# Performance work log

Hardware: AMD Instinct MI355X
Metric: run time of the kernel (lower is better)

The kernel has to match this reference:

```python
import jax, jax.numpy as jnp
import numpy as np

B, T = 8, 1024
C_IN, C_H = 4096, 4096
K_I, K_H = 3, 3
INIT_SPARSITY = 0.15


def _fixed_fanin_bipartite(rng, n_out, n_in, k):
    # exactly k True entries per row, distinct columns
    r = rng.random((n_out, n_in))
    cols = np.argsort(r, axis=1)[:, :k]
    A = np.zeros((n_out, n_in), np.float32)
    np.put_along_axis(A, cols, 1.0, axis=1)
    return A


def _fixed_fanin_graph(rng, n, k):
    # exactly k True entries per row, distinct non-self columns
    r = rng.random((n, n))
    np.fill_diagonal(r, 2.0)  # exclude self-loops
    cols = np.argsort(r, axis=1)[:, :k]
    A = np.zeros((n, n), np.float32)
    np.put_along_axis(A, cols, 1.0, axis=1)
    return A


def setup_inputs() -> dict:
    rng = np.random.default_rng(0)
    z = jnp.asarray(rng.random((B, T, C_IN)) < INIT_SPARSITY)          # bool (B,T,C_in)
    h0 = jnp.asarray(rng.random((B, C_H)) < INIT_SPARSITY)             # bool (B,C_h)
    A_input_f = jnp.asarray(_fixed_fanin_bipartite(rng, C_H, C_IN, K_I))  # (C_h,C_in) f32
    A_hidden_f = jnp.asarray(_fixed_fanin_graph(rng, C_H, K_H))           # (C_h,C_h) f32
    return {"z": z, "h0": h0, "A_input_f": A_input_f, "A_hidden_f": A_hidden_f}


def reference(z, h0, A_input_f, A_hidden_f):
    # AND-of-ORs CA: h_i(t) = [OR over input fan-in of z(t)] AND [OR over hidden fan-in of h(t-1)]
    z_tf = jnp.moveaxis(z, -2, 0)  # (T, B, C_in)

    def step(h, z_t):
        input_or = (z_t.astype(jnp.float32) @ A_input_f.T) > 0   # (B, C_h) bool
        hidden_or = (h.astype(jnp.float32) @ A_hidden_f.T) > 0   # (B, C_h) bool
        h_new = input_or & hidden_or
        return h_new, h_new

    _, h_seq = jax.lax.scan(step, h0, z_tf)   # (T, B, C_h)
    h_seq = jnp.moveaxis(h_seq, 0, -2)        # (B, T, C_h)
    return jnp.concatenate([z, h_seq], axis=-1)  # (B, T, C_in + C_h) bool
```

## Files before the change

### kernel.cpp

```cpp
#include <hip/hip_runtime.h>
#include <stdint.h>

#define B_   8
#define T_   1024
#define CIN_ 4096
#define CH_  4096
#define GRP  16
#define NGRP (T_ / GRP)


__device__ __forceinline__ uint32_t bytes_nonzero01(uint32_t w) {
  uint32_t t = (w & 0x7F7F7F7Fu) + 0x7F7F7F7Fu;
  t = (t | w) & 0x80808080u;
  return t >> 7;
}

__device__ __forceinline__ uint32_t load4(const void* base, long idx4, int es) {
  if (es == 1) {
    uint32_t w = ((const uint32_t*)base)[idx4];
    return bytes_nonzero01(w);
  } else if (es == 2) {
    uint32_t w0 = ((const uint32_t*)base)[idx4 * 2];
    uint32_t w1 = ((const uint32_t*)base)[idx4 * 2 + 1];
    uint32_t r = 0;
    r |= ((w0 & 0xFFFFu) != 0u) ? 0x00000001u : 0u;
    r |= ((w0 >> 16)     != 0u) ? 0x00000100u : 0u;
    r |= ((w1 & 0xFFFFu) != 0u) ? 0x00010000u : 0u;
    r |= ((w1 >> 16)     != 0u) ? 0x01000000u : 0u;
    return r;
  } else {
    uint4 w = ((const uint4*)base)[idx4];
    uint32_t r = 0;
    r |= (w.x != 0u) ? 0x00000001u : 0u;
    r |= (w.y != 0u) ? 0x00000100u : 0u;
    r |= (w.z != 0u) ? 0x00010000u : 0u;
    r |= (w.w != 0u) ? 0x01000000u : 0u;
    return r;
  }
}

__device__ __forceinline__ uint4 expand01(uint32_t v4) {
  uint4 r = { v4 & 1u, (v4 >> 8) & 1u, (v4 >> 16) & 1u, (v4 >> 24) & 1u };
  return r;
}

__device__ __forceinline__ void wait_ge(uint32_t* p, uint32_t tgt) {
  while (__hip_atomic_load(p, __ATOMIC_RELAXED, __HIP_MEMORY_SCOPE_AGENT) < tgt)
    __builtin_amdgcn_s_sleep(2);
  __threadfence();
}
__device__ __forceinline__ void bump(uint32_t* p) {
  __threadfence();
  __hip_atomic_fetch_add(p, 1u, __ATOMIC_RELAXED, __HIP_MEMORY_SCOPE_AGENT);
}

#define BID_DETECT 8
#define BID_EXTIN0 9
#define BID_EXTH0  265
#define BID_INOR0  521
#define NBLK       (521 + T_)

__global__ __launch_bounds__(1024) void mega_kernel(const void* __restrict__ z,
                                                    const void* __restrict__ h0,
                                                    const float* __restrict__ Ain,
                                                    const float* __restrict__ Ah,
                                                    uint32_t* __restrict__ modep,
                                                    uint32_t* __restrict__ idxin,
                                                    uint32_t* __restrict__ idxh,
                                                    uint32_t* __restrict__ inorb,
                                                    uint32_t* __restrict__ flags,
                                                    uint32_t* __restrict__ out) {
  __shared__ __align__(16) unsigned char smem[88 * 1024];
  unsigned char* sm0 = &smem[0];
  unsigned char* sm1 = &smem[4096];
  int* scnt = (int*)&smem[8192];
  const int bid = blockIdx.x;
  const int n = threadIdx.x;

  if (bid < 8) {
    __builtin_amdgcn_s_setprio(1);
    const int b = bid;
    if (n == 0) wait_ge(&flags[0], 1);
    __syncthreads();
    const int es = (int)modep[0];
    ((uint32_t*)sm0)[n] = load4(h0, (long)b * 1024 + n, es);
    if (n == 0) wait_ge(&flags[2], 256);
    __syncthreads();
    uint32_t d[4][3];
    {
      const uint4* p = (const uint4*)(idxh + n * 12);
      uint4 q0 = p[0], q1 = p[1], q2 = p[2];
      d[0][0] = q0.x; d[0][1] = q0.y; d[0][2] = q0.z;
      d[1][0] = q0.w; d[1][1] = q1.x; d[1][2] = q1.y;
      d[2][0] = q1.z; d[2][1] = q1.w; d[2][2] = q2.x;
      d[3][0] = q2.y; d[3][1] = q2.z; d[3][2] = q2.w;
    }
    __syncthreads();
    uint32_t* outh = out + (long)b * T_ * 8192 + 4096;
    int p = 0;
    for (int g = 0; g < NGRP; ++g) {
      if (n == 0) wait_ge(&flags[8 + g], GRP);
      __syncthreads();
      uint32_t inw = inorb[(g * GRP) * 1024 + n];
      for (int tt = 0; tt < GRP; ++tt) {
        const int t = g * GRP + tt;
        uint32_t inw_next = (tt < GRP - 1) ? inorb[(t + 1) * 1024 + n] : 0u;
        const unsigned char* hc = p ? sm1 : sm0;
        unsigned char* hn = p ? sm0 : sm1;
        uint32_t mask = (inw >> b) & 0x01010101u;
        uint32_t o4 = 0;
        if (mask) {
          if (mask & 0x00000001u) { uint32_t v = (uint32_t)hc[d[0][0]] | hc[d[0][1]] | hc[d[0][2]]; o4 |= v; }
          if (mask & 0x00000100u) { uint32_t v = (uint32_t)hc[d[1][0]] | hc[d[1][1]] | hc[d[1][2]]; o4 |= v << 8; }
          if (mask & 0x00010000u) { uint32_t v = (uint32_t)hc[d[2][0]] | hc[d[2][1]] | hc[d[2][2]]; o4 |= v << 16; }
          if (mask & 0x01000000u) { uint32_t v = (uint32_t)hc[d[3][0]] | hc[d[3][1]] | hc[d[3][2]]; o4 |= v << 24; }
        }
        ((uint32_t*)hn)[n] = o4;
        ((uint4*)(outh + (long)t * 8192))[n] = expand01(o4);
        __syncthreads();
        inw = inw_next;
        p ^= 1;
      }
    }
    return;
  }

  if (bid == BID_DETECT) {
    if (n == 0) { scnt[0] = 1; scnt[1] = 1; scnt[2] = 1; scnt[3] = 0; }
    __syncthreads();
    {
      const uint32_t* zw = (const uint32_t*)z;
      int okB = 1, okH = 1, okW = 1, low = 0;
      #pragma unroll
      for (int k = 0; k < 4; ++k) {
        uint32_t w = zw[n + 1024 * k];
        if ((w & 0xFEFEFEFEu) != 0u) okB = 0;
        uint32_t lo = w & 0xFFFFu, hi = w >> 16;
        if (!((lo == 0u || lo == 0x3F80u) && (hi == 0u || hi == 0x3F80u))) okH = 0;
        if (!(w == 0u || w == 1u)) okW = 0;
        if (lo != 0u) low = 1;
      }
      if (!okB) atomicAnd(&scnt[0], 0);
      if (!okH) atomicAnd(&scnt[1], 0);
      if (!okW) atomicAnd(&scnt[2], 0);
      if (low)  atomicOr(&scnt[3], 1);
    }
    __syncthreads();
    if (n == 0) {
      uint32_t mode;
      if (scnt[2])      mode = 4;
      else if (scnt[0]) mode = 1;
      else if (scnt[1]) mode = scnt[3] ? 2 : 4;
      else              mode = 1;
      modep[0] = mode;
      bump(&flags[0]);
    }
    return;
  }

  if (bid < BID_INOR0) {
    const int isIn = (bid < BID_EXTH0);
    const int eb = isIn ? (bid - BID_EXTIN0) : (bid - BID_EXTH0);
    const int wave = n >> 6, lane = n & 63;
    const int row = eb * 16 + wave;
    const float* A = (isIn ? Ain : Ah) + (long)row * 4096;
    uint32_t* outp = (isIn ? idxin : idxh) + row * 3;
    if (lane == 0) scnt[wave] = 0;
    __syncthreads();
    const float4* A4 = (const float4*)A;
    #pragma unroll
    for (int it = 0; it < 16; ++it) {
      float4 v = A4[it * 64 + lane];
      int cbase = (it * 64 + lane) * 4;
      if (v.x != 0.0f) { int q = atomicAdd(&scnt[wave], 1); if (q < 3) outp[q] = cbase;     }
      if (v.y != 0.0f) { int q = atomicAdd(&scnt[wave], 1); if (q < 3) outp[q] = cbase + 1; }
      if (v.z != 0.0f) { int q = atomicAdd(&scnt[wave], 1); if (q < 3) outp[q] = cbase + 2; }
      if (v.w != 0.0f) { int q = atomicAdd(&scnt[wave], 1); if (q < 3) outp[q] = cbase + 3; }
    }
    __syncthreads();
    if (n == 0) bump(isIn ? &flags[1] : &flags[2]);
    return;
  }

  {
    const int t = bid - BID_INOR0;
    if (n == 0) { wait_ge(&flags[0], 1); wait_ge(&flags[1], 256); }
    __syncthreads();
    const int es = (int)modep[0];
    uint32_t acc = 0;
    #pragma unroll
    for (int b = 0; b < B_; ++b) {
      uint32_t v4 = load4(z, ((long)b * T_ + t) * 1024 + n, es);
      acc |= v4 << b;
      ((uint4*)(out + ((long)b * T_ + t) * 8192))[n] = expand01(v4);
    }
    ((uint32_t*)sm0)[n] = acc;
    __syncthreads();
    const unsigned char* zp = sm0;
    const uint4* ip = (const uint4*)(idxin + n * 12);
    uint4 q0 = ip[0], q1 = ip[1], q2 = ip[2];
    uint32_t r0 = (uint32_t)zp[q0.x] | zp[q0.y] | zp[q0.z];
    uint32_t r1 = (uint32_t)zp[q0.w] | zp[q1.x] | zp[q1.y];
    uint32_t r2 = (uint32_t)zp[q1.z] | zp[q1.w] | zp[q2.x];
    uint32_t r3 = (uint32_t)zp[q2.y] | zp[q2.z] | zp[q2.w];
    inorb[t * 1024 + n] = r0 | (r1 << 8) | (r2 << 16) | (r3 << 24);
    __syncthreads();
    if (n == 0) bump(&flags[8 + (t >> 4)]);
    return;
  }
}

extern "C" void kernel_launch(void* const* d_in, const int* in_sizes, int n_in,
                              void* d_out, int out_size, void* d_ws, size_t ws_size,
                              hipStream_t stream) {
  const void*  z   = d_in[0];
  const void*  h0  = d_in[1];
  const float* Ain = (const float*)d_in[2];
  const float* Ah  = (const float*)d_in[3];
  uint32_t* out = (uint32_t*)d_out;

  char* ws = (char*)d_ws;
  uint32_t* modep = (uint32_t*)(ws);
  uint32_t* idxin = (uint32_t*)(ws + 256);
  uint32_t* idxh  = (uint32_t*)(ws + 256 + 49152);
  uint32_t* inorb = (uint32_t*)(ws + 98560);
  uint32_t* flagp = (uint32_t*)(ws + 4292864);

  hipMemsetAsync(flagp, 0, 4096, stream);
  mega_kernel<<<NBLK, 1024, 0, stream>>>(z, h0, Ain, Ah, modep, idxin, idxh,
                                         inorb, flagp, out);
}
```

Baseline: 1.127 ms.

## Run scan in one bit-packed block with persistent work-queue workers and deferred expansion

The eight per-batch scan blocks are merged into a single block that handles all batches at once, keeping the eight batch bits packed in each byte and computing the hidden step branch-free, ANDed with the input-OR word. The scan now writes a compact packed hidden sequence, and the expansion of h to the output is moved into separate tasks that other blocks pick up through an atomic work queue. The launch becomes a persistent grid of 256 blocks pulling tasks in dependency order, and the flag-clearing memset is replaced by a tiny kernel. The aim is to shorten the serial critical path and take the large output writes off it, at the cost of an extra workspace round trip for the hidden sequence and extra flag synchronisation.

```diff
diff --git a/kernel.cpp b/kernel.cpp
--- a/kernel.cpp
+++ b/kernel.cpp
@@ -7,6 +7,20 @@
 #define CH_  4096
 #define GRP  16
 #define NGRP (T_ / GRP)
+
+#define TK_DETECT 0
+#define TK_EXTIN0 1
+#define TK_EXTH0  257
+#define TK_INOR0  513
+#define TK_EXP0   1537
+#define TK_END    2561
+
+#define F_MODE 0
+#define F_EXIN 1
+#define F_EXH  2
+#define F_INOR 8
+#define F_SCAN 128
+#define F_QCTR 200
 
 
 __device__ __forceinline__ uint32_t bytes_nonzero01(uint32_t w) {
@@ -54,11 +68,9 @@
   __hip_atomic_fetch_add(p, 1u, __ATOMIC_RELAXED, __HIP_MEMORY_SCOPE_AGENT);
 }
 
-#define BID_DETECT 8
-#define BID_EXTIN0 9
-#define BID_EXTH0  265
-#define BID_INOR0  521
-#define NBLK       (521 + T_)
+__global__ __launch_bounds__(256) void zero_kernel(uint32_t* __restrict__ f) {
+  f[threadIdx.x] = 0;
+}
 
 __global__ __launch_bounds__(1024) void mega_kernel(const void* __restrict__ z,
                                                     const void* __restrict__ h0,
@@ -68,23 +80,26 @@
                                                     uint32_t* __restrict__ idxin,
                                                     uint32_t* __restrict__ idxh,
                                                     uint32_t* __restrict__ inorb,
+                                                    uint32_t* __restrict__ hseq,
                                                     uint32_t* __restrict__ flags,
                                                     uint32_t* __restrict__ out) {
   __shared__ __align__(16) unsigned char smem[88 * 1024];
   unsigned char* sm0 = &smem[0];
   unsigned char* sm1 = &smem[4096];
   int* scnt = (int*)&smem[8192];
-  const int bid = blockIdx.x;
+  __shared__ int tsk;
   const int n = threadIdx.x;
 
-  if (bid < 8) {
+  if (blockIdx.x == 0) {
     __builtin_amdgcn_s_setprio(1);
-    const int b = bid;
-    if (n == 0) wait_ge(&flags[0], 1);
+    if (n == 0) wait_ge(&flags[F_MODE], 1);
     __syncthreads();
     const int es = (int)modep[0];
-    ((uint32_t*)sm0)[n] = load4(h0, (long)b * 1024 + n, es);
-    if (n == 0) wait_ge(&flags[2], 256);
+    uint32_t acc = 0;
+    #pragma unroll
+    for (int b = 0; b < B_; ++b) acc |= load4(h0, (long)b * 1024 + n, es) << b;
+    ((uint32_t*)sm0)[n] = acc;
+    if (n == 0) wait_ge(&flags[F_EXH], 256);
     __syncthreads();
     uint32_t d[4][3];
     {
@@ -96,10 +111,9 @@
       d[3][0] = q2.y; d[3][1] = q2.z; d[3][2] = q2.w;
     }
     __syncthreads();
-    uint32_t* outh = out + (long)b * T_ * 8192 + 4096;
     int p = 0;
     for (int g = 0; g < NGRP; ++g) {
-      if (n == 0) wait_ge(&flags[8 + g], GRP);
+      if (n == 0) wait_ge(&flags[F_INOR + g], GRP);
       __syncthreads();
       uint32_t inw = inorb[(g * GRP) * 1024 + n];
       for (int tt = 0; tt < GRP; ++tt) {
@@ -107,28 +121,34 @@
         uint32_t inw_next = (tt < GRP - 1) ? inorb[(t + 1) * 1024 + n] : 0u;
         const unsigned char* hc = p ? sm1 : sm0;
         unsigned char* hn = p ? sm0 : sm1;
-        uint32_t mask = (inw >> b) & 0x01010101u;
-        uint32_t o4 = 0;
-        if (mask) {
-          if (mask & 0x00000001u) { uint32_t v = (uint32_t)hc[d[0][0]] | hc[d[0][1]] | hc[d[0][2]]; o4 |= v; }
-          if (mask & 0x00000100u) { uint32_t v = (uint32_t)hc[d[1][0]] | hc[d[1][1]] | hc[d[1][2]]; o4 |= v << 8; }
-          if (mask & 0x00010000u) { uint32_t v = (uint32_t)hc[d[2][0]] | hc[d[2][1]] | hc[d[2][2]]; o4 |= v << 16; }
-          if (mask & 0x01000000u) { uint32_t v = (uint32_t)hc[d[3][0]] | hc[d[3][1]] | hc[d[3][2]]; o4 |= v << 24; }
-        }
+        uint32_t v0 = (uint32_t)hc[d[0][0]] | hc[d[0][1]] | hc[d[0][2]];
+        uint32_t v1 = (uint32_t)hc[d[1][0]] | hc[d[1][1]] | hc[d[1][2]];
+        uint32_t v2 = (uint32_t)hc[d[2][0]] | hc[d[2][1]] | hc[d[2][2]];
+        uint32_t v3 = (uint32_t)hc[d[3][0]] | hc[d[3][1]] | hc[d[3][2]];
+        uint32_t o4 = (v0 | (v1 << 8) | (v2 << 16) | (v3 << 24)) & inw;
         ((uint32_t*)hn)[n] = o4;
-        ((uint4*)(outh + (long)t * 8192))[n] = expand01(o4);
+        hseq[(size_t)t * 1024 + n] = o4;
         __syncthreads();
         inw = inw_next;
         p ^= 1;
       }
+      if (n == 0) bump(&flags[F_SCAN + g]);
     }
     return;
   }
 
-  if (bid == BID_DETECT) {
-    if (n == 0) { scnt[0] = 1; scnt[1] = 1; scnt[2] = 1; scnt[3] = 0; }
-    __syncthreads();
-    {
+  uint32_t* qctr = &flags[F_QCTR];
+  for (;;) {
+    __syncthreads();
+    if (n == 0) tsk = (int)__hip_atomic_fetch_add(qctr, 1u, __ATOMIC_RELAXED,
+                                                  __HIP_MEMORY_SCOPE_AGENT);
+    __syncthreads();
+    const int task = tsk;
+    if (task >= TK_END) return;
+
+    if (task == TK_DETECT) {
+      if (n == 0) { scnt[0] = 1; scnt[1] = 1; scnt[2] = 1; scnt[3] = 0; }
+      __syncthreads();
       const uint32_t* zw = (const uint32_t*)z;
       int okB = 1, okH = 1, okW = 1, low = 0;
       #pragma unroll
@@ -144,69 +164,81 @@
       if (!okH) atomicAnd(&scnt[1], 0);
       if (!okW) atomicAnd(&scnt[2], 0);
       if (low)  atomicOr(&scnt[3], 1);
-    }
-    __syncthreads();
-    if (n == 0) {
-      uint32_t mode;
-      if (scnt[2])      mode = 4;
-      else if (scnt[0]) mode = 1;
-      else if (scnt[1]) mode = scnt[3] ? 2 : 4;
-      else              mode = 1;
-      modep[0] = mode;
-      bump(&flags[0]);
-    }
-    return;
-  }
-
-  if (bid < BID_INOR0) {
-    const int isIn = (bid < BID_EXTH0);
-    const int eb = isIn ? (bid - BID_EXTIN0) : (bid - BID_EXTH0);
-    const int wave = n >> 6, lane = n & 63;
-    const int row = eb * 16 + wave;
-    const float* A = (isIn ? Ain : Ah) + (long)row * 4096;
-    uint32_t* outp = (isIn ? idxin : idxh) + row * 3;
-    if (lane == 0) scnt[wave] = 0;
-    __syncthreads();
-    const float4* A4 = (const float4*)A;
-    #pragma unroll
-    for (int it = 0; it < 16; ++it) {
-      float4 v = A4[it * 64 + lane];
-      int cbase = (it * 64 + lane) * 4;
-      if (v.x != 0.0f) { int q = atomicAdd(&scnt[wave], 1); if (q < 3) outp[q] = cbase;     }
-      if (v.y != 0.0f) { int q = atomicAdd(&scnt[wave], 1); if (q < 3) outp[q] = cbase + 1; }
-      if (v.z != 0.0f) { int q = atomicAdd(&scnt[wave], 1); if (q < 3) outp[q] = cbase + 2; }
-      if (v.w != 0.0f) { int q = atomicAdd(&scnt[wave], 1); if (q < 3) outp[q] = cbase + 3; }
-    }
-    __syncthreads();
-    if (n == 0) bump(isIn ? &flags[1] : &flags[2]);
-    return;
-  }
-
-  {
-    const int t = bid - BID_INOR0;
-    if (n == 0) { wait_ge(&flags[0], 1); wait_ge(&flags[1], 256); }
-    __syncthreads();
-    const int es = (int)modep[0];
-    uint32_t acc = 0;
-    #pragma unroll
-    for (int b = 0; b < B_; ++b) {
-      uint32_t v4 = load4(z, ((long)b * T_ + t) * 1024 + n, es);
-      acc |= v4 << b;
-      ((uint4*)(out + ((long)b * T_ + t) * 8192))[n] = expand01(v4);
-    }
-    ((uint32_t*)sm0)[n] = acc;
-    __syncthreads();
-    const unsigned char* zp = sm0;
-    const uint4* ip = (const uint4*)(idxin + n * 12);
-    uint4 q0 = ip[0], q1 = ip[1], q2 = ip[2];
-    uint32_t r0 = (uint32_t)zp[q0.x] | zp[q0.y] | zp[q0.z];
-    uint32_t r1 = (uint32_t)zp[q0.w] | zp[q1.x] | zp[q1.y];
-    uint32_t r2 = (uint32_t)zp[q1.z] | zp[q1.w] | zp[q2.x];
-    uint32_t r3 = (uint32_t)zp[q2.y] | zp[q2.z] | zp[q2.w];
-    inorb[t * 1024 + n] = r0 | (r1 << 8) | (r2 << 16) | (r3 << 24);
-    __syncthreads();
-    if (n == 0) bump(&flags[8 + (t >> 4)]);
-    return;
+      __syncthreads();
+      if (n == 0) {
+        uint32_t mode;
+        if (scnt[2])      mode = 4;
+        else if (scnt[0]) mode = 1;
+        else if (scnt[1]) mode = scnt[3] ? 2 : 4;
+        else              mode = 1;
+        modep[0] = mode;
+        bump(&flags[F_MODE]);
+      }
+      continue;
+    }
+
+    if (task < TK_INOR0) {
+      const int isIn = (task < TK_EXTH0);
+      const int eb = task - (isIn ? TK_EXTIN0 : TK_EXTH0);
+      const int wave = n >> 6, lane = n & 63;
+      const int row = eb * 16 + wave;
+      const float* A = (isIn ? Ain : Ah) + (long)row * 4096;
+      uint32_t* outp = (isIn ? idxin : idxh) + row * 3;
+      if (lane == 0) scnt[wave] = 0;
+      __syncthreads();
+      const float4* A4 = (const float4*)A;
+      #pragma unroll
+      for (int it = 0; it < 16; ++it) {
+        float4 v = A4[it * 64 + lane];
+        int cbase = (it * 64 + lane) * 4;
+        if (v.x != 0.0f) { int q = atomicAdd(&scnt[wave], 1); if (q < 3) outp[q] = cbase;     }
+        if (v.y != 0.0f) { int q = atomicAdd(&scnt[wave], 1); if (q < 3) outp[q] = cbase + 1; }
+        if (v.z != 0.0f) { int q = atomicAdd(&scnt[wave], 1); if (q < 3) outp[q] = cbase + 2; }
+        if (v.w != 0.0f) { int q = atomicAdd(&scnt[wave], 1); if (q < 3) outp[q] = cbase + 3; }
+      }
+      __syncthreads();
+      if (n == 0) bump(isIn ? &flags[F_EXIN] : &flags[F_EXH]);
+      continue;
+    }
+
+    if (task < TK_EXP0) {
+      const int t = task - TK_INOR0;
+      if (n == 0) { wait_ge(&flags[F_MODE], 1); wait_ge(&flags[F_EXIN], 256); }
+      __syncthreads();
+      const int es = (int)modep[0];
+      uint32_t acc = 0;
+      #pragma unroll
+      for (int b = 0; b < B_; ++b) {
+        uint32_t v4 = load4(z, ((long)b * T_ + t) * 1024 + n, es);
+        acc |= v4 << b;
+        ((uint4*)(out + ((long)b * T_ + t) * 8192))[n] = expand01(v4);
+      }
+      ((uint32_t*)sm0)[n] = acc;
+      __syncthreads();
+      const unsigned char* zp = sm0;
+      const uint4* ip = (const uint4*)(idxin + n * 12);
+      uint4 q0 = ip[0], q1 = ip[1], q2 = ip[2];
+      uint32_t r0 = (uint32_t)zp[q0.x] | zp[q0.y] | zp[q0.z];
+      uint32_t r1 = (uint32_t)zp[q0.w] | zp[q1.x] | zp[q1.y];
+      uint32_t r2 = (uint32_t)zp[q1.z] | zp[q1.w] | zp[q2.x];
+      uint32_t r3 = (uint32_t)zp[q2.y] | zp[q2.z] | zp[q2.w];
+      inorb[t * 1024 + n] = r0 | (r1 << 8) | (r2 << 16) | (r3 << 24);
+      __syncthreads();
+      if (n == 0) bump(&flags[F_INOR + (t >> 4)]);
+      continue;
+    }
+
+    {
+      const int t = task - TK_EXP0;
+      if (n == 0) wait_ge(&flags[F_SCAN + (t >> 4)], 1);
+      __syncthreads();
+      const uint32_t w = hseq[(size_t)t * 1024 + n];
+      #pragma unroll
+      for (int b = 0; b < B_; ++b)
+        ((uint4*)(out + ((long)b * T_ + t) * 8192 + 4096))[n] =
+            expand01((w >> b) & 0x01010101u);
+      continue;
+    }
   }
 }
 
@@ -225,8 +257,9 @@
   uint32_t* idxh  = (uint32_t*)(ws + 256 + 49152);
   uint32_t* inorb = (uint32_t*)(ws + 98560);
   uint32_t* flagp = (uint32_t*)(ws + 4292864);
-
-  hipMemsetAsync(flagp, 0, 4096, stream);
-  mega_kernel<<<NBLK, 1024, 0, stream>>>(z, h0, Ain, Ah, modep, idxin, idxh,
-                                         inorb, flagp, out);
-}
+  uint32_t* hseq  = (uint32_t*)(ws + 4293888);
+
+  zero_kernel<<<1, 256, 0, stream>>>(flagp);
+  mega_kernel<<<256, 1024, 0, stream>>>(z, h0, Ain, Ah, modep, idxin, idxh,
+                                        inorb, hseq, flagp, out);
+}
```

After: 1.280 ms. 1.14x slower.
